# Kernel optimization log

Measured on AMD Instinct MI355X. Metric: run time of the kernel, lower is better.

The kernel has to match this reference:

```python
import jax, jax.numpy as jnp
import numpy as np

N_NODES = 50000
N_EDGES = 600000
IN_DIM = 128
HID = 256
OUT = 3


def setup_inputs() -> dict:
    key = jax.random.key(0)
    ks = jax.random.split(key, 10)
    x = jax.random.normal(ks[0], (N_NODES, IN_DIM), dtype=jnp.float32)
    edge_index = jax.random.randint(ks[1], (2, N_EDGES), 0, N_NODES, dtype=jnp.int64)
    s = lambda k, shp: jax.random.normal(k, shp, dtype=jnp.float32) * (1.0 / np.sqrt(shp[0]))
    return {
        "x": x,
        "edge_index": edge_index,
        # SAGEConv1: lin_l (applied to aggregated neighbors, with bias), lin_r (root, no bias)
        "W1l": s(ks[2], (IN_DIM, HID)), "b1": jnp.zeros((HID,), jnp.float32), "W1r": s(ks[3], (IN_DIM, HID)),
        # SAGEConv2
        "W2l": s(ks[4], (HID, HID)), "b2": jnp.zeros((HID,), jnp.float32), "W2r": s(ks[5], (HID, HID)),
        # classification head
        "Wh": s(ks[6], (HID, OUT)), "bh": jnp.zeros((OUT,), jnp.float32),
    }


def _sage_conv(x, edge_index, Wl, b, Wr):
    """PyG SAGEConv with mean aggregation: out = lin_l(mean_{j->i} x_j) + lin_r(x_i)."""
    src, dst = edge_index[0], edge_index[1]
    n = x.shape[0]
    # gather source features and scatter-mean onto targets
    msg_sum = jax.ops.segment_sum(x[src], dst, num_segments=n)          # [N, d]
    deg = jax.ops.segment_sum(jnp.ones((src.shape[0],), x.dtype), dst, num_segments=n)
    mean = msg_sum / jnp.maximum(deg, 1.0)[:, None]                      # isolated nodes -> 0
    return mean @ Wl + b + x @ Wr


def reference(x, edge_index, W1l, b1, W1r, W2l, b2, W2r, Wh, bh):
    h = jax.nn.relu(_sage_conv(x, edge_index, W1l, b1, W1r))
    # dropout(p=0.2) is identity in eval mode
    h = jax.nn.relu(_sage_conv(h, edge_index, W2l, b2, W2r))
    return h @ Wh + bh
```

## Files before the change

### kernel.cpp

```cpp
#include <hip/hip_runtime.h>
#include <hip/hip_bf16.h>

#define N_NODES 50000
#define N_EDGES 600000
#define IN_DIM 128
#define HID 256
#define OUT_DIM 3

#define M_PAD 50048
#define N_PANELS 391

#define SCAN_B 256
#define SCAN_NB ((N_NODES + SCAN_B - 1) / SCAN_B)

typedef __bf16 bf16x8 __attribute__((ext_vector_type(8)));
typedef float f32x4 __attribute__((ext_vector_type(4)));

static __device__ __forceinline__ unsigned short f2b(float f) {
    union { float f; unsigned u; } u; u.f = f;
    unsigned r = u.u + 0x7fffu + ((u.u >> 16) & 1u);
    return (unsigned short)(r >> 16);
}
static __device__ __forceinline__ float b2f(unsigned short b) {
    union { unsigned u; float f; } u; u.u = ((unsigned)b) << 16;
    return u.f;
}

static __device__ __forceinline__ size_t swz(int r, int k, int K) {
    return (((size_t)((r >> 4) * (K >> 5) + (k >> 5))) << 9)
         + ((((k >> 3) & 3) * 16 + (r & 15)) << 3) + (k & 7);
}


__global__ void count_deg_kernel(const int* __restrict__ dst, int* __restrict__ counts) {
    int e = blockIdx.x * blockDim.x + threadIdx.x;
    if (e < N_EDGES) atomicAdd(&counts[dst[e]], 1);
}

__global__ __launch_bounds__(256) void block_sum_kernel(const int* __restrict__ counts,
                                                        int* __restrict__ partial) {
    int node = blockIdx.x * SCAN_B + threadIdx.x;
    int v = (node < N_NODES) ? counts[node] : 0;
#pragma unroll
    for (int off = 32; off > 0; off >>= 1) v += __shfl_down(v, off);
    __shared__ int ws[4];
    if ((threadIdx.x & 63) == 0) ws[threadIdx.x >> 6] = v;
    __syncthreads();
    if (threadIdx.x == 0) partial[blockIdx.x] = ws[0] + ws[1] + ws[2] + ws[3];
}

__global__ __launch_bounds__(256) void scan_partial_kernel(int* __restrict__ partial) {
    __shared__ int s[SCAN_B];
    int t = threadIdx.x;
    int v = (t < SCAN_NB) ? partial[t] : 0;
    s[t] = v;
    __syncthreads();
    for (int off = 1; off < SCAN_B; off <<= 1) {
        int u = (t >= off) ? s[t - off] : 0;
        __syncthreads();
        s[t] += u;
        __syncthreads();
    }
    if (t < SCAN_NB) partial[t] = s[t] - v;
}

__global__ __launch_bounds__(256) void write_rowptr_kernel(const int* __restrict__ counts,
                                                           const int* __restrict__ partial,
                                                           int* __restrict__ row_ptr) {
    __shared__ int s[SCAN_B];
    int t = threadIdx.x;
    int node = blockIdx.x * SCAN_B + t;
    int v = (node < N_NODES) ? counts[node] : 0;
    s[t] = v;
    __syncthreads();
    for (int off = 1; off < SCAN_B; off <<= 1) {
        int u = (t >= off) ? s[t - off] : 0;
        __syncthreads();
        s[t] += u;
        __syncthreads();
    }
    if (node < N_NODES) row_ptr[node] = partial[blockIdx.x] + s[t] - v;
    if (node == 0) row_ptr[N_NODES] = N_EDGES;
}

__global__ void fill_csr_kernel(const int* __restrict__ src, const int* __restrict__ dst,
                                const int* __restrict__ row_ptr, int* __restrict__ cursor,
                                int* __restrict__ csr_src) {
    int e = blockIdx.x * blockDim.x + threadIdx.x;
    if (e < N_EDGES) {
        int d = dst[e];
        int pos = atomicAdd(&cursor[d], 1);
        csr_src[row_ptr[d] + pos] = src[e];
    }
}


__global__ void cast_f2b_kernel(const float* __restrict__ in,
                                unsigned short* __restrict__ out_row,
                                unsigned short* __restrict__ out_swz) {
    int i = blockIdx.x * blockDim.x + threadIdx.x;
    if (i * 4 < N_NODES * IN_DIM) {
        float4 v = ((const float4*)in)[i];
        ushort4 o;
        o.x = f2b(v.x); o.y = f2b(v.y); o.z = f2b(v.z); o.w = f2b(v.w);
        ((ushort4*)out_row)[i] = o;
        int m = i >> 5;
        int kb = (i & 31) * 4;
        *(ushort4*)(out_swz + swz(m, kb, IN_DIM)) = o;
    }
}

__global__ void tcast4_kernel(const float* __restrict__ W1l, const float* __restrict__ W1r,
                              const float* __restrict__ W2l, const float* __restrict__ W2r,
                              unsigned short* __restrict__ W1lt, unsigned short* __restrict__ W1rt,
                              unsigned short* __restrict__ W2lt, unsigned short* __restrict__ W2rt) {
    int i = blockIdx.x * blockDim.x + threadIdx.x;
    const float* in; unsigned short* out; int K, base;
    if (i < 32768)        { in = W1l; out = W1lt; K = IN_DIM; base = 0; }
    else if (i < 65536)   { in = W1r; out = W1rt; K = IN_DIM; base = 32768; }
    else if (i < 131072)  { in = W2l; out = W2lt; K = HID;    base = 65536; }
    else if (i < 196608)  { in = W2r; out = W2rt; K = HID;    base = 131072; }
    else return;
    int j = i - base;
    int k = j >> 8;
    int n = j & 255;
    out[swz(n, k, K)] = f2b(in[j]);
}

__global__ void init_out_kernel(const float* __restrict__ bh, float* __restrict__ out) {
    int i = blockIdx.x * blockDim.x + threadIdx.x;
    if (i < N_NODES * 3) out[i] = bh[i % 3];
}


static __device__ __forceinline__ void addv(float* acc, uint4 v) {
    acc[0] += b2f((unsigned short)(v.x & 0xffff));
    acc[1] += b2f((unsigned short)(v.x >> 16));
    acc[2] += b2f((unsigned short)(v.y & 0xffff));
    acc[3] += b2f((unsigned short)(v.y >> 16));
    acc[4] += b2f((unsigned short)(v.z & 0xffff));
    acc[5] += b2f((unsigned short)(v.z >> 16));
    acc[6] += b2f((unsigned short)(v.w & 0xffff));
    acc[7] += b2f((unsigned short)(v.w >> 16));
}

static __device__ __forceinline__ uint4 pack8(const float* a) {
    uint4 pk;
    pk.x = (unsigned)f2b(a[0]) | ((unsigned)f2b(a[1]) << 16);
    pk.y = (unsigned)f2b(a[2]) | ((unsigned)f2b(a[3]) << 16);
    pk.z = (unsigned)f2b(a[4]) | ((unsigned)f2b(a[5]) << 16);
    pk.w = (unsigned)f2b(a[6]) | ((unsigned)f2b(a[7]) << 16);
    return pk;
}

__global__ __launch_bounds__(256) void agg_mean256_kernel(const unsigned short* __restrict__ feat,
                                                          const int* __restrict__ row_ptr,
                                                          const int* __restrict__ csr_src,
                                                          unsigned short* __restrict__ out_swz) {
    int node = blockIdx.x * 4 + (threadIdx.x >> 6);
    if (node >= N_NODES) return;
    int lane = threadIdx.x & 63;
    int half = lane >> 5, lh = lane & 31;
    const uint4* f4 = (const uint4*)feat;
    float acc[8];
#pragma unroll
    for (int j = 0; j < 8; j++) acc[j] = 0.f;
    int beg = row_ptr[node], end = row_ptr[node + 1];
    int i = beg;
    for (; i + 4 <= end; i += 4) {
        int sA = csr_src[i + half];
        int sB = csr_src[i + 2 + half];
        uint4 vA = f4[(size_t)sA * 32 + lh];
        uint4 vB = f4[(size_t)sB * 32 + lh];
        addv(acc, vA);
        addv(acc, vB);
    }
    if (i + 2 <= end) {
        int s = csr_src[i + half];
        addv(acc, f4[(size_t)s * 32 + lh]);
        i += 2;
    }
    if (i < end && half == 0) {
        int s = csr_src[i];
        addv(acc, f4[(size_t)s * 32 + lh]);
    }
    float inv = (end > beg) ? 1.0f / (float)(end - beg) : 0.0f;
#pragma unroll
    for (int j = 0; j < 8; j++) {
        acc[j] += __shfl_xor(acc[j], 32);
        acc[j] *= inv;
    }
    if (half == 0) *(uint4*)(out_swz + swz(node, lh * 8, HID)) = pack8(acc);
}

__global__ __launch_bounds__(256) void agg_mean128_kernel(const unsigned short* __restrict__ feat,
                                                          const int* __restrict__ row_ptr,
                                                          const int* __restrict__ csr_src,
                                                          unsigned short* __restrict__ out_swz) {
    int node = blockIdx.x * 4 + (threadIdx.x >> 6);
    if (node >= N_NODES) return;
    int lane = threadIdx.x & 63;
    int q = lane >> 4, lq = lane & 15;
    const uint4* f4 = (const uint4*)feat;
    float acc[8];
#pragma unroll
    for (int j = 0; j < 8; j++) acc[j] = 0.f;
    int beg = row_ptr[node], end = row_ptr[node + 1];
    int i = beg;
    for (; i + 8 <= end; i += 8) {
        int sA = csr_src[i + q];
        int sB = csr_src[i + 4 + q];
        uint4 vA = f4[(size_t)sA * 16 + lq];
        uint4 vB = f4[(size_t)sB * 16 + lq];
        addv(acc, vA);
        addv(acc, vB);
    }
    if (i + 4 <= end) {
        int s = csr_src[i + q];
        addv(acc, f4[(size_t)s * 16 + lq]);
        i += 4;
    }
    int rem = end - i;
    if (q < rem) {
        int s = csr_src[i + q];
        addv(acc, f4[(size_t)s * 16 + lq]);
    }
    float inv = (end > beg) ? 1.0f / (float)(end - beg) : 0.0f;
#pragma unroll
    for (int j = 0; j < 8; j++) {
        acc[j] += __shfl_xor(acc[j], 32);
        acc[j] += __shfl_xor(acc[j], 16);
        acc[j] *= inv;
    }
    if (q == 0) *(uint4*)(out_swz + swz(node, lq * 8, IN_DIM)) = pack8(acc);
}


template <int KP>
static __device__ __forceinline__ void gemm_swz_core_pd4(
    const unsigned short* __restrict__ A0, const unsigned short* __restrict__ B0,
    const unsigned short* __restrict__ A1, const unsigned short* __restrict__ B1,
    int tmw, int tn0, int l, f32x4 (&acc)[2][4]) {
    constexpr int KT = KP / 32;
    constexpr int TT = 2 * KT;
    bf16x8 a[4][2], b[4][4];

    auto ldtile = [&](int t_, int s_) {
        const unsigned short* A_ = (t_ < KT) ? A0 : A1;
        const unsigned short* B_ = (t_ < KT) ? B0 : B1;
        const int tk_ = (t_ < KT) ? t_ : t_ - KT;
        a[s_][0] = *(const bf16x8*)(A_ + ((((size_t)tmw) * KT + tk_) << 9) + l * 8);
        a[s_][1] = *(const bf16x8*)(A_ + ((((size_t)(tmw + 1)) * KT + tk_) << 9) + l * 8);
#pragma unroll
        for (int nt = 0; nt < 4; nt++)
            b[s_][nt] = *(const bf16x8*)(B_ + ((((size_t)(tn0 + nt)) * KT + tk_) << 9) + l * 8);
    };

#pragma unroll
    for (int p = 0; p < 3; p++) ldtile(p, p);
#pragma unroll
    for (int t = 0; t < TT; t++) {
        const int cur = t & 3;
        if (t + 3 < TT) ldtile(t + 3, (t + 3) & 3);
#pragma unroll
        for (int mt = 0; mt < 2; mt++)
#pragma unroll
            for (int nt = 0; nt < 4; nt++)
                acc[mt][nt] = __builtin_amdgcn_mfma_f32_16x16x32_bf16(a[cur][mt], b[cur][nt],
                                                                      acc[mt][nt], 0, 0, 0);
    }
}

template <int KP>
__global__ __launch_bounds__(256, 3) void gemm_swz_kernel(
    const unsigned short* __restrict__ A0, const unsigned short* __restrict__ B0,
    const unsigned short* __restrict__ A1, const unsigned short* __restrict__ B1,
    const float* __restrict__ bias, unsigned short* __restrict__ out_row,
    unsigned short* __restrict__ out_swz, int M) {
    const int bid = blockIdx.x;
    const int panel = (bid >> 5) * 8 + (bid & 7);
    if (panel >= N_PANELS) return;
    const int t = threadIdx.x;
    const int w = t >> 6, l = t & 63;
    const int quad = l >> 4, lr = l & 15;
    const int m0 = panel * 128, n0 = ((bid >> 3) & 3) * 64;
    const int tmw = (m0 >> 4) + w * 2, tn0 = n0 >> 4;

    f32x4 acc[2][4];
    const f32x4 zero = {0.f, 0.f, 0.f, 0.f};
#pragma unroll
    for (int mt = 0; mt < 2; mt++)
#pragma unroll
        for (int nt = 0; nt < 4; nt++) acc[mt][nt] = zero;

    float bias_r[4];
#pragma unroll
    for (int nt = 0; nt < 4; nt++) bias_r[nt] = bias[n0 + nt * 16 + lr];

    gemm_swz_core_pd4<KP>(A0, B0, A1, B1, tmw, tn0, l, acc);

#pragma unroll
    for (int mt = 0; mt < 2; mt++)
#pragma unroll
        for (int r = 0; r < 4; r++) {
            int gm = m0 + w * 32 + mt * 16 + quad * 4 + r;
            if (gm >= M) continue;
            unsigned short* orow = out_row + (size_t)gm * HID;
#pragma unroll
            for (int nt = 0; nt < 4; nt++) {
                int gn = n0 + nt * 16 + lr;
                unsigned short h = f2b(fmaxf(acc[mt][nt][r] + bias_r[nt], 0.f));
                orow[gn] = h;
                out_swz[swz(gm, gn, HID)] = h;
            }
        }
}

template <int KP>
__global__ __launch_bounds__(256, 3) void gemm_swz_head_kernel(
    const unsigned short* __restrict__ A0, const unsigned short* __restrict__ B0,
    const unsigned short* __restrict__ A1, const unsigned short* __restrict__ B1,
    const float* __restrict__ bias, const float* __restrict__ Wh,
    float* __restrict__ out, int M) {
    const int bid = blockIdx.x;
    const int panel = (bid >> 5) * 8 + (bid & 7);
    if (panel >= N_PANELS) return;
    const int t = threadIdx.x;
    const int w = t >> 6, l = t & 63;
    const int quad = l >> 4, lr = l & 15;
    const int m0 = panel * 128, n0 = ((bid >> 3) & 3) * 64;
    const int tmw = (m0 >> 4) + w * 2, tn0 = n0 >> 4;

    f32x4 acc[2][4];
    const f32x4 zero = {0.f, 0.f, 0.f, 0.f};
#pragma unroll
    for (int mt = 0; mt < 2; mt++)
#pragma unroll
        for (int nt = 0; nt < 4; nt++) acc[mt][nt] = zero;

    float bias_r[4];
    float wh_r[4][3];
#pragma unroll
    for (int nt = 0; nt < 4; nt++) {
        int gn = n0 + nt * 16 + lr;
        bias_r[nt] = bias[gn];
        wh_r[nt][0] = Wh[gn * 3 + 0];
        wh_r[nt][1] = Wh[gn * 3 + 1];
        wh_r[nt][2] = Wh[gn * 3 + 2];
    }

    gemm_swz_core_pd4<KP>(A0, B0, A1, B1, tmw, tn0, l, acc);

#pragma unroll
    for (int mt = 0; mt < 2; mt++)
#pragma unroll
        for (int r = 0; r < 4; r++) {
            int gm = m0 + w * 32 + mt * 16 + quad * 4 + r;
            float p0 = 0.f, p1 = 0.f, p2 = 0.f;
#pragma unroll
            for (int nt = 0; nt < 4; nt++) {
                float v = fmaxf(acc[mt][nt][r] + bias_r[nt], 0.f);
                p0 += v * wh_r[nt][0];
                p1 += v * wh_r[nt][1];
                p2 += v * wh_r[nt][2];
            }
#pragma unroll
            for (int off = 1; off < 16; off <<= 1) {
                p0 += __shfl_xor(p0, off);
                p1 += __shfl_xor(p1, off);
                p2 += __shfl_xor(p2, off);
            }
            if (lr == 0 && gm < M) {
                atomicAdd(&out[(size_t)gm * 3 + 0], p0);
                atomicAdd(&out[(size_t)gm * 3 + 1], p1);
                atomicAdd(&out[(size_t)gm * 3 + 2], p2);
            }
        }
}


extern "C" void kernel_launch(void* const* d_in, const int* in_sizes, int n_in,
                              void* d_out, int out_size, void* d_ws, size_t ws_size,
                              hipStream_t stream) {
    const float* x   = (const float*)d_in[0];
    const int*   ei  = (const int*)d_in[1];
    const int*   src = ei;
    const int*   dst = ei + N_EDGES;
    const float* W1l = (const float*)d_in[2];
    const float* b1  = (const float*)d_in[3];
    const float* W1r = (const float*)d_in[4];
    const float* W2l = (const float*)d_in[5];
    const float* b2  = (const float*)d_in[6];
    const float* W2r = (const float*)d_in[7];
    const float* Wh  = (const float*)d_in[8];
    const float* bh  = (const float*)d_in[9];
    float* out = (float*)d_out;

    char* ws = (char*)d_ws;
    size_t off = 0;
    auto alloc = [&](size_t bytes) -> void* {
        void* p = ws + off;
        off = (off + bytes + 255) & ~(size_t)255;
        return p;
    };
    int* counts   = (int*)alloc((size_t)N_NODES * 4);
    int* row_ptr  = (int*)alloc((size_t)(N_NODES + 1) * 4);
    int* cursor   = (int*)alloc((size_t)N_NODES * 4);
    int* partial  = (int*)alloc((size_t)SCAN_NB * 4);
    int* csr_src  = (int*)alloc((size_t)N_EDGES * 4);
    unsigned short* xb_row  = (unsigned short*)alloc((size_t)M_PAD * IN_DIM * 2);
    unsigned short* xb_swz  = (unsigned short*)alloc((size_t)M_PAD * IN_DIM * 2);
    unsigned short* agg1    = (unsigned short*)alloc((size_t)M_PAD * IN_DIM * 2);
    unsigned short* h1_row  = (unsigned short*)alloc((size_t)M_PAD * HID * 2);
    unsigned short* h1_swz  = (unsigned short*)alloc((size_t)M_PAD * HID * 2);
    unsigned short* agg2    = (unsigned short*)alloc((size_t)M_PAD * HID * 2);
    unsigned short* W1lt = (unsigned short*)alloc((size_t)IN_DIM * HID * 2);
    unsigned short* W1rt = (unsigned short*)alloc((size_t)IN_DIM * HID * 2);
    unsigned short* W2lt = (unsigned short*)alloc((size_t)HID * HID * 2);
    unsigned short* W2rt = (unsigned short*)alloc((size_t)HID * HID * 2);

    hipMemsetAsync(counts, 0, (size_t)N_NODES * 4, stream);
    hipMemsetAsync(cursor, 0, (size_t)N_NODES * 4, stream);

    const int eblocks = (N_EDGES + 255) / 256;
    count_deg_kernel<<<eblocks, 256, 0, stream>>>(dst, counts);
    block_sum_kernel<<<SCAN_NB, SCAN_B, 0, stream>>>(counts, partial);
    scan_partial_kernel<<<1, SCAN_B, 0, stream>>>(partial);
    write_rowptr_kernel<<<SCAN_NB, SCAN_B, 0, stream>>>(counts, partial, row_ptr);
    fill_csr_kernel<<<eblocks, 256, 0, stream>>>(src, dst, row_ptr, cursor, csr_src);

    {
        int n = N_NODES * IN_DIM;
        cast_f2b_kernel<<<(n / 4 + 255) / 256, 256, 0, stream>>>(x, xb_row, xb_swz);
        tcast4_kernel<<<(196608 + 255) / 256, 256, 0, stream>>>(W1l, W1r, W2l, W2r,
                                                                W1lt, W1rt, W2lt, W2rt);
        init_out_kernel<<<(N_NODES * 3 + 255) / 256, 256, 0, stream>>>(bh, out);
    }

    const int nblocks4 = (N_NODES + 3) / 4;
    const int gemm_blocks = ((N_PANELS + 7) / 8) * 32;

    agg_mean128_kernel<<<nblocks4, 256, 0, stream>>>(xb_row, row_ptr, csr_src, agg1);
    gemm_swz_kernel<IN_DIM><<<gemm_blocks, 256, 0, stream>>>(agg1, W1lt, xb_swz, W1rt, b1,
                                                             h1_row, h1_swz, N_NODES);

    agg_mean256_kernel<<<nblocks4, 256, 0, stream>>>(h1_row, row_ptr, csr_src, agg2);
    gemm_swz_head_kernel<HID><<<gemm_blocks, 256, 0, stream>>>(agg2, W2lt, h1_swz, W2rt, b2, Wh,
                                                               out, N_NODES);
}
```

Baseline: 302.1 us.

## Stage GEMM weight tiles in LDS and merge prep casts into one kernel

The two SAGE GEMM kernels now copy the block's 64-column weight panel into shared memory once per operand pair, and read B fragments from LDS instead of each wave loading them from global memory. The A-side keeps its 3-deep register prefetch, but B prefetching is gone and a __syncthreads is added between the two operand passes, and the launch_bounds occupancy hint is dropped. Separately, the x cast, weight transpose-cast and output bias init kernels are fused into one prep kernel to save launches. The LDS staging removes redundant global/L2 reads of B across the four waves, at the cost of a serialized load phase and up to 32KB of shared memory per block.

```diff
diff --git a/kernel.cpp b/kernel.cpp
--- a/kernel.cpp
+++ b/kernel.cpp
@@ -95,41 +95,42 @@
 }
 
 
-__global__ void cast_f2b_kernel(const float* __restrict__ in,
-                                unsigned short* __restrict__ out_row,
-                                unsigned short* __restrict__ out_swz) {
+#define PREP_X (N_NODES * IN_DIM / 4)
+#define PREP_W (PREP_X + 196608)
+#define PREP_O (PREP_W + N_NODES * 3)
+
+__global__ void prep_kernel(const float* __restrict__ x,
+                            const float* __restrict__ W1l, const float* __restrict__ W1r,
+                            const float* __restrict__ W2l, const float* __restrict__ W2r,
+                            const float* __restrict__ bh,
+                            unsigned short* __restrict__ xb_row,
+                            unsigned short* __restrict__ xb_swz,
+                            unsigned short* __restrict__ W1lt, unsigned short* __restrict__ W1rt,
+                            unsigned short* __restrict__ W2lt, unsigned short* __restrict__ W2rt,
+                            float* __restrict__ out) {
     int i = blockIdx.x * blockDim.x + threadIdx.x;
-    if (i * 4 < N_NODES * IN_DIM) {
-        float4 v = ((const float4*)in)[i];
+    if (i < PREP_X) {
+        float4 v = ((const float4*)x)[i];
         ushort4 o;
         o.x = f2b(v.x); o.y = f2b(v.y); o.z = f2b(v.z); o.w = f2b(v.w);
-        ((ushort4*)out_row)[i] = o;
+        ((ushort4*)xb_row)[i] = o;
         int m = i >> 5;
         int kb = (i & 31) * 4;
-        *(ushort4*)(out_swz + swz(m, kb, IN_DIM)) = o;
-    }
-}
-
-__global__ void tcast4_kernel(const float* __restrict__ W1l, const float* __restrict__ W1r,
-                              const float* __restrict__ W2l, const float* __restrict__ W2r,
-                              unsigned short* __restrict__ W1lt, unsigned short* __restrict__ W1rt,
-                              unsigned short* __restrict__ W2lt, unsigned short* __restrict__ W2rt) {
-    int i = blockIdx.x * blockDim.x + threadIdx.x;
-    const float* in; unsigned short* out; int K, base;
-    if (i < 32768)        { in = W1l; out = W1lt; K = IN_DIM; base = 0; }
-    else if (i < 65536)   { in = W1r; out = W1rt; K = IN_DIM; base = 32768; }
-    else if (i < 131072)  { in = W2l; out = W2lt; K = HID;    base = 65536; }
-    else if (i < 196608)  { in = W2r; out = W2rt; K = HID;    base = 131072; }
-    else return;
-    int j = i - base;
-    int k = j >> 8;
-    int n = j & 255;
-    out[swz(n, k, K)] = f2b(in[j]);
-}
-
-__global__ void init_out_kernel(const float* __restrict__ bh, float* __restrict__ out) {
-    int i = blockIdx.x * blockDim.x + threadIdx.x;
-    if (i < N_NODES * 3) out[i] = bh[i % 3];
+        *(ushort4*)(xb_swz + swz(m, kb, IN_DIM)) = o;
+    } else if (i < PREP_W) {
+        int j = i - PREP_X;
+        const float* in; unsigned short* outw; int K;
+        if (j < 32768)       { in = W1l; outw = W1lt; K = IN_DIM; }
+        else if (j < 65536)  { in = W1r; outw = W1rt; K = IN_DIM; j -= 32768; }
+        else if (j < 131072) { in = W2l; outw = W2lt; K = HID;    j -= 65536; }
+        else                 { in = W2r; outw = W2rt; K = HID;    j -= 131072; }
+        int k = j >> 8;
+        int n = j & 255;
+        outw[swz(n, k, K)] = f2b(in[j]);
+    } else if (i < PREP_O) {
+        int j = i - PREP_W;
+        out[j] = bh[j % 3];
+    }
 }
 
 
@@ -237,46 +238,58 @@
 
 
 template <int KP>
-static __device__ __forceinline__ void gemm_swz_core_pd4(
+static __device__ __forceinline__ void gemm_lds_core(
     const unsigned short* __restrict__ A0, const unsigned short* __restrict__ B0,
     const unsigned short* __restrict__ A1, const unsigned short* __restrict__ B1,
-    int tmw, int tn0, int l, f32x4 (&acc)[2][4]) {
+    unsigned short* Bl,
+    int tmw, int tn0, int t, int l, f32x4 (&acc)[2][4]) {
     constexpr int KT = KP / 32;
-    constexpr int TT = 2 * KT;
-    bf16x8 a[4][2], b[4][4];
-
-    auto ldtile = [&](int t_, int s_) {
-        const unsigned short* A_ = (t_ < KT) ? A0 : A1;
-        const unsigned short* B_ = (t_ < KT) ? B0 : B1;
-        const int tk_ = (t_ < KT) ? t_ : t_ - KT;
-        a[s_][0] = *(const bf16x8*)(A_ + ((((size_t)tmw) * KT + tk_) << 9) + l * 8);
-        a[s_][1] = *(const bf16x8*)(A_ + ((((size_t)(tmw + 1)) * KT + tk_) << 9) + l * 8);
-#pragma unroll
-        for (int nt = 0; nt < 4; nt++)
-            b[s_][nt] = *(const bf16x8*)(B_ + ((((size_t)(tn0 + nt)) * KT + tk_) << 9) + l * 8);
-    };
-
-#pragma unroll
-    for (int p = 0; p < 3; p++) ldtile(p, p);
-#pragma unroll
-    for (int t = 0; t < TT; t++) {
-        const int cur = t & 3;
-        if (t + 3 < TT) ldtile(t + 3, (t + 3) & 3);
-#pragma unroll
-        for (int mt = 0; mt < 2; mt++)
+
+    for (int p = 0; p < 2; p++) {
+        const unsigned short* A = p ? A1 : A0;
+        const unsigned short* B = p ? B1 : B0;
+        if (p) __syncthreads();
+        {
+            const uint4* srcp = (const uint4*)(B + (((size_t)tn0 * KT) << 9));
+            uint4* dstp = (uint4*)Bl;
+            constexpr int TOT = 4 * KT * 64;
+#pragma unroll
+            for (int i = 0; i < TOT / 256; i++) dstp[i * 256 + t] = srcp[i * 256 + t];
+        }
+        __syncthreads();
+
+        bf16x8 a[4][2];
+        auto lda = [&](int tk, int s) {
+            a[s][0] = *(const bf16x8*)(A + ((((size_t)tmw) * KT + tk) << 9) + l * 8);
+            a[s][1] = *(const bf16x8*)(A + ((((size_t)(tmw + 1)) * KT + tk) << 9) + l * 8);
+        };
+#pragma unroll
+        for (int q = 0; q < 3 && q < KT; q++) lda(q, q);
+#pragma unroll
+        for (int tk = 0; tk < KT; tk++) {
+            const int cur = tk & 3;
+            if (tk + 3 < KT) lda(tk + 3, (tk + 3) & 3);
+            bf16x8 b[4];
 #pragma unroll
             for (int nt = 0; nt < 4; nt++)
-                acc[mt][nt] = __builtin_amdgcn_mfma_f32_16x16x32_bf16(a[cur][mt], b[cur][nt],
-                                                                      acc[mt][nt], 0, 0, 0);
+                b[nt] = *(const bf16x8*)&Bl[((((size_t)nt) * KT + tk) << 9) + l * 8];
+#pragma unroll
+            for (int mt = 0; mt < 2; mt++)
+#pragma unroll
+                for (int nt = 0; nt < 4; nt++)
+                    acc[mt][nt] = __builtin_amdgcn_mfma_f32_16x16x32_bf16(a[cur][mt], b[nt],
+                                                                          acc[mt][nt], 0, 0, 0);
+        }
     }
 }
 
 template <int KP>
-__global__ __launch_bounds__(256, 3) void gemm_swz_kernel(
+__global__ __launch_bounds__(256) void gemm_lds_kernel(
     const unsigned short* __restrict__ A0, const unsigned short* __restrict__ B0,
     const unsigned short* __restrict__ A1, const unsigned short* __restrict__ B1,
     const float* __restrict__ bias, unsigned short* __restrict__ out_row,
     unsigned short* __restrict__ out_swz, int M) {
+    __shared__ __align__(16) unsigned short Bl[64 * KP];
     const int bid = blockIdx.x;
     const int panel = (bid >> 5) * 8 + (bid & 7);
     if (panel >= N_PANELS) return;
@@ -297,7 +310,7 @@
 #pragma unroll
     for (int nt = 0; nt < 4; nt++) bias_r[nt] = bias[n0 + nt * 16 + lr];
 
-    gemm_swz_core_pd4<KP>(A0, B0, A1, B1, tmw, tn0, l, acc);
+    gemm_lds_core<KP>(A0, B0, A1, B1, Bl, tmw, tn0, t, l, acc);
 
 #pragma unroll
     for (int mt = 0; mt < 2; mt++)
@@ -317,11 +330,12 @@
 }
 
 template <int KP>
-__global__ __launch_bounds__(256, 3) void gemm_swz_head_kernel(
+__global__ __launch_bounds__(256) void gemm_lds_head_kernel(
     const unsigned short* __restrict__ A0, const unsigned short* __restrict__ B0,
     const unsigned short* __restrict__ A1, const unsigned short* __restrict__ B1,
     const float* __restrict__ bias, const float* __restrict__ Wh,
     float* __restrict__ out, int M) {
+    __shared__ __align__(16) unsigned short Bl[64 * KP];
     const int bid = blockIdx.x;
     const int panel = (bid >> 5) * 8 + (bid & 7);
     if (panel >= N_PANELS) return;
@@ -349,7 +363,7 @@
         wh_r[nt][2] = Wh[gn * 3 + 2];
     }
 
-    gemm_swz_core_pd4<KP>(A0, B0, A1, B1, tmw, tn0, l, acc);
+    gemm_lds_core<KP>(A0, B0, A1, B1, Bl, tmw, tn0, t, l, acc);
 
 #pragma unroll
     for (int mt = 0; mt < 2; mt++)
@@ -429,22 +443,18 @@
     write_rowptr_kernel<<<SCAN_NB, SCAN_B, 0, stream>>>(counts, partial, row_ptr);
     fill_csr_kernel<<<eblocks, 256, 0, stream>>>(src, dst, row_ptr, cursor, csr_src);
 
-    {
-        int n = N_NODES * IN_DIM;
-        cast_f2b_kernel<<<(n / 4 + 255) / 256, 256, 0, stream>>>(x, xb_row, xb_swz);
-        tcast4_kernel<<<(196608 + 255) / 256, 256, 0, stream>>>(W1l, W1r, W2l, W2r,
-                                                                W1lt, W1rt, W2lt, W2rt);
-        init_out_kernel<<<(N_NODES * 3 + 255) / 256, 256, 0, stream>>>(bh, out);
-    }
+    prep_kernel<<<(PREP_O + 255) / 256, 256, 0, stream>>>(x, W1l, W1r, W2l, W2r, bh,
+                                                          xb_row, xb_swz,
+                                                          W1lt, W1rt, W2lt, W2rt, out);
 
     const int nblocks4 = (N_NODES + 3) / 4;
     const int gemm_blocks = ((N_PANELS + 7) / 8) * 32;
 
     agg_mean128_kernel<<<nblocks4, 256, 0, stream>>>(xb_row, row_ptr, csr_src, agg1);
-    gemm_swz_kernel<IN_DIM><<<gemm_blocks, 256, 0, stream>>>(agg1, W1lt, xb_swz, W1rt, b1,
+    gemm_lds_kernel<IN_DIM><<<gemm_blocks, 256, 0, stream>>>(agg1, W1lt, xb_swz, W1rt, b1,
                                                              h1_row, h1_swz, N_NODES);
 
     agg_mean256_kernel<<<nblocks4, 256, 0, stream>>>(h1_row, row_ptr, csr_src, agg2);
-    gemm_swz_head_kernel<HID><<<gemm_blocks, 256, 0, stream>>>(agg2, W2lt, h1_swz, W2rt, b2, Wh,
+    gemm_lds_head_kernel<HID><<<gemm_blocks, 256, 0, stream>>>(agg2, W2lt, h1_swz, W2rt, b2, Wh,
                                                                out, N_NODES);
 }
```

New measurement: 298.3 us. No clear change (-1.3%).
